# Optimization experiments

Hardware: AMD Instinct MI355X
Metric: run time of the kernel (lower is better)

The kernel has to match this reference:

```python
import jax, jax.numpy as jnp
import numpy as np

L, B, E = 8192, 2, 1024
H, WS = 16, 256
D = E // H


def setup_inputs() -> dict:
    key = jax.random.key(0)
    ks = jax.random.split(key, 8)
    mk = lambda k: jax.random.normal(k, (E, E), dtype=jnp.float32) * 0.02
    return {
        'query': jax.random.normal(ks[0], (L, B, E), dtype=jnp.float32),
        'key':   jax.random.normal(ks[1], (L, B, E), dtype=jnp.float32),
        'value': jax.random.normal(ks[2], (L, B, E), dtype=jnp.float32),
        'Wq': mk(ks[3]), 'bq': jnp.zeros((E,), jnp.float32),
        'Wk': mk(ks[4]), 'bk': jnp.zeros((E,), jnp.float32),
        'Wv': mk(ks[5]), 'bv': jnp.zeros((E,), jnp.float32),
        'Wo': mk(ks[6]), 'bo': jnp.zeros((E,), jnp.float32),
    }


def reference(query, key, value, Wq, bq, Wk, bk, Wv, bv, Wo, bo):
    # Faithful translation, including the original's (B,L,H,D) layout and the
    # raw-memory view(B,H,L//ws,ws,D) reinterpretation of that layout.
    proj = lambda x, W, b: x @ W.T + b
    # (L,B,E) -> (L,B,H,D) -> transpose(0,1) -> (B,L,H,D)
    q = jnp.swapaxes(proj(query, Wq, bq).reshape(L, B, H, D), 0, 1)
    k = jnp.swapaxes(proj(key,   Wk, bk).reshape(L, B, H, D), 0, 1)
    v = jnp.swapaxes(proj(value, Wv, bv).reshape(L, B, H, D), 0, 1)
    # L > ws, L % ws == 0 -> pad_len = 0; contiguous().view == reshape
    nW = L // WS
    q = q.reshape(B, H, nW, WS, D)
    k = k.reshape(B, H, nW, WS, D)
    v = v.reshape(B, H, nW, WS, D)
    attn = jnp.einsum('bhnqd,bhnkd->bhnqk', q, k) / (D ** 0.5)
    attn = jax.nn.softmax(attn, axis=-1)
    out = jnp.einsum('bhnqk,bhnkd->bhnqd', attn, v)  # (B,H,nW,ws,D)
    out = out.reshape(B, H, L, D)
    # transpose(0,1).contiguous().view(L,B,E): reinterpret (H,B,L,D) memory
    out = jnp.swapaxes(out, 0, 1).reshape(L, B, E)
    return out @ Wo.T + bo
```

## Files before the change

kernel.cpp:

```cpp
#include <hip/hip_runtime.h>


typedef _Float16 half8 __attribute__((ext_vector_type(8)));
typedef _Float16 half4 __attribute__((ext_vector_type(4)));
typedef float    f32x4 __attribute__((ext_vector_type(4)));

#define MFMA16(a, b, c) __builtin_amdgcn_mfma_f32_16x16x32_f16((a), (b), (c), 0, 0, 0)
#define VM(n) asm volatile("s_waitcnt vmcnt(" #n ")" ::: "memory")
#define SCHED0 __builtin_amdgcn_sched_barrier(0)
#define LGKM0 do { asm volatile("s_waitcnt lgkmcnt(0)" ::: "memory"); SCHED0; } while (0)
#define BARW do { __builtin_amdgcn_s_barrier(); SCHED0; } while (0)

__device__ inline void gload16(const _Float16* g, _Float16* l) {
  __builtin_amdgcn_global_load_lds(
      (const __attribute__((address_space(1))) void*)g,
      (__attribute__((address_space(3))) void*)l, 16, 0, 0);
}

__device__ inline half8 cvt8(float4 a, float4 b) {
  half8 h = {(_Float16)a.x, (_Float16)a.y, (_Float16)a.z, (_Float16)a.w,
             (_Float16)b.x, (_Float16)b.y, (_Float16)b.z, (_Float16)b.w};
  return h;
}

__global__ __launch_bounds__(256) void cvt_fp16_k(const float* __restrict__ src,
                                                  _Float16* __restrict__ dst, int n) {
  int i = (blockIdx.x * 256 + threadIdx.x) * 8;
  if (i >= n) return;
  float4 a = *(const float4*)(src + i);
  float4 b = *(const float4*)(src + i + 4);
  *(half8*)(dst + i) = cvt8(a, b);
}

__global__ __launch_bounds__(256) void cvtw_k(const float* __restrict__ s0,
                                              const float* __restrict__ s1,
                                              const float* __restrict__ s2,
                                              const float* __restrict__ s3,
                                              _Float16* __restrict__ d) {
  const float* s = blockIdx.y == 0 ? s0 : blockIdx.y == 1 ? s1 : blockIdx.y == 2 ? s2 : s3;
  _Float16* dst = d + (size_t)blockIdx.y * (1 << 20);
  int i = (blockIdx.x * 256 + threadIdx.x) * 8;
  float4 a = *(const float4*)(s + i);
  float4 b = *(const float4*)(s + i + 4);
  *(half8*)(dst + i) = cvt8(a, b);
}

template <int OUT_F32>
__global__ __launch_bounds__(512) void gemm8p_k(const _Float16* __restrict__ Ah,
                                                const _Float16* __restrict__ Bw,
                                                const float* __restrict__ bias,
                                                void* __restrict__ Cout, float scale) {
  constexpr int K = 1024, NN = 1024, NT = 16;
  __shared__ alignas(16) _Float16 SH[65536];
  const int tid = threadIdx.x, lane = tid & 63, wave = tid >> 6;
  const int r15 = lane & 15, g = lane >> 4;
  const int wr = wave >> 2, wc = wave & 3;
  const int m0 = blockIdx.x * 256, n0 = blockIdx.y * 256;

  const int sp = tid >> 3;
  const int sv = (tid & 7) ^ (sp & 7);
  const int srow = 2 * sp + (sv >> 2);
  const int scol = (sv & 3) * 8;
  const int sdst = tid * 8;

  const int rp = r15 >> 1, rsub = r15 & 1;
  const int rslot = ((rsub * 4 + g) ^ rp) * 8;

  f32x4 acc[8][4] = {};
  half8 af[4], bf[4];

#define A_REGION(buf, kh) (&SH[(buf)*16384 + (kh)*8192])
#define B_REGION(buf, kh) (&SH[32768 + (buf)*16384 + (kh)*8192])

#define STAGE_B(t, buf, kh)                                                    \
  do {                                                                         \
    const _Float16* _s = Bw + (size_t)(n0 + srow) * K + (t)*64 + (kh)*32 + scol; \
    gload16(_s, B_REGION(buf, kh) + sdst);                                     \
    gload16(_s + (size_t)128 * K, B_REGION(buf, kh) + sdst + 4096);            \
  } while (0)

#define STAGE_A16(t, buf, kh)                                                  \
  do {                                                                         \
    const _Float16* _s = Ah + (size_t)(m0 + srow) * K + (t)*64 + (kh)*32 + scol; \
    gload16(_s, A_REGION(buf, kh) + sdst);                                     \
    gload16(_s + (size_t)128 * K, A_REGION(buf, kh) + sdst + 4096);            \
  } while (0)

#define READ_AF(buf, kk, MH)                                                   \
  do {                                                                         \
    _Float16* _b = A_REGION(buf, kk);                                          \
    int _pb = (wr * 64 + (MH)*32 + rp) * 64 + rslot;                           \
    af[0] = *(half8*)&_b[_pb];                                                 \
    af[1] = *(half8*)&_b[_pb + 512];                                           \
    af[2] = *(half8*)&_b[_pb + 1024];                                          \
    af[3] = *(half8*)&_b[_pb + 1536];                                          \
  } while (0)

#define READ_BF(buf, kk)                                                       \
  do {                                                                         \
    _Float16* _b = B_REGION(buf, kk);                                          \
    int _pb = (wc * 32 + rp) * 64 + rslot;                                     \
    bf[0] = *(half8*)&_b[_pb];                                                 \
    bf[1] = *(half8*)&_b[_pb + 512];                                           \
    bf[2] = *(half8*)&_b[_pb + 1024];                                          \
    bf[3] = *(half8*)&_b[_pb + 1536];                                          \
  } while (0)

#define MFMA_Q(MH)                                                             \
  do {                                                                         \
    __builtin_amdgcn_s_setprio(1);                                             \
    _Pragma("unroll") for (int mi = 0; mi < 4; mi++)                           \
        _Pragma("unroll") for (int ni = 0; ni < 4; ni++) acc[(MH)*4 + mi][ni] = \
        MFMA16(af[mi], bf[ni], acc[(MH)*4 + mi][ni]);                          \
    __builtin_amdgcn_s_setprio(0);                                             \
  } while (0)

  STAGE_A16(0, 0, 0);
  STAGE_A16(0, 0, 1);
  STAGE_B(0, 0, 0);
  STAGE_B(0, 0, 1);

  for (int t = 0; t < NT - 1; t++) {
    const int buf = t & 1, nb = buf ^ 1;
    STAGE_A16(t + 1, nb, 0);
    VM(4);
    SCHED0; BARW;
    READ_AF(buf, 0, 0);
    READ_BF(buf, 0);
    LGKM0;
    MFMA_Q(0);
    STAGE_A16(t + 1, nb, 1);
    READ_AF(buf, 0, 1);
    LGKM0;
    MFMA_Q(1);
    STAGE_B(t + 1, nb, 0);
    VM(6);
    SCHED0; BARW;
    READ_AF(buf, 1, 0);
    READ_BF(buf, 1);
    LGKM0;
    MFMA_Q(0);
    STAGE_B(t + 1, nb, 1);
    READ_AF(buf, 1, 1);
    LGKM0;
    MFMA_Q(1);
  }
  {
    VM(2);
    SCHED0; BARW;
    READ_AF(1, 0, 0);
    READ_BF(1, 0);
    LGKM0;
    MFMA_Q(0);
    READ_AF(1, 0, 1);
    LGKM0;
    MFMA_Q(1);
    VM(0);
    SCHED0; BARW;
    READ_AF(1, 1, 0);
    READ_BF(1, 1);
    LGKM0;
    MFMA_Q(0);
    READ_AF(1, 1, 1);
    LGKM0;
    MFMA_Q(1);
  }

#pragma unroll
  for (int ni = 0; ni < 4; ni++) {
    const int col = n0 + wc * 64 + ni * 16 + r15;
    const float bv = bias[col];
#pragma unroll
    for (int mi8 = 0; mi8 < 8; mi8++) {
      const int rowb = m0 + wr * 128 + mi8 * 16 + g * 4;
#pragma unroll
      for (int r = 0; r < 4; r++) {
        float x = (acc[mi8][ni][r] + bv) * scale;
        if (OUT_F32)
          ((float*)Cout)[(size_t)(rowb + r) * NN + col] = x;
        else
          ((_Float16*)Cout)[(size_t)(rowb + r) * NN + col] = (_Float16)x;
      }
    }
  }
#undef A_REGION
#undef B_REGION
#undef STAGE_B
#undef STAGE_A16
#undef READ_AF
#undef READ_BF
#undef MFMA_Q
}

__global__ __launch_bounds__(256) void vtrans_k(const _Float16* __restrict__ Vp,
                                                _Float16* __restrict__ Vt) {
  const int c = blockIdx.x, b = blockIdx.y;
  __shared__ alignas(16) _Float16 Vl[256 * 64];
  const int tid = threadIdx.x;
  const int l0 = c * 16;
#pragma unroll
  for (int i = 0; i < 8; i++) {
    int q = tid + i * 256;
    int w = q >> 3, ck = q & 7;
    int ls = l0 + (w >> 4), h = w & 15;
    half8 v = *(const half8*)(Vp + (size_t)(ls * 2 + b) * 1024 + h * 64 + ck * 8);
    *(half8*)&Vl[w * 64 + (ck ^ (w & 7)) * 8] = v;
  }
  __syncthreads();
  const int d = tid >> 2, kcq = tid & 3;
  const size_t obase = ((size_t)(b * 512 + c) * 64 + d) * 256 + kcq * 64;
#pragma unroll
  for (int i8 = 0; i8 < 8; i8++) {
    half8 v;
#pragma unroll
    for (int j = 0; j < 8; j++) {
      int k = kcq * 64 + i8 * 8 + j;
      v[j] = Vl[k * 64 + (((d >> 3) ^ (k & 7)) * 8) + (d & 7)];
    }
    *(half8*)(Vt + obase + i8 * 8) = v;
  }
}

__global__ __launch_bounds__(512) void attn_win_k(const _Float16* __restrict__ Qp,
                                                  const _Float16* __restrict__ Kp,
                                                  const _Float16* __restrict__ Vt,
                                                  _Float16* __restrict__ Y) {
  const int c = blockIdx.x, b = blockIdx.y;
  __shared__ alignas(16) _Float16 Kl[256 * 64];
  __shared__ alignas(16) _Float16 Vl[64 * 256];
  const int tid = threadIdx.x, lane = tid & 63, wave = tid >> 6;
  const int i15 = lane & 15, g = lane >> 4;
  const int l0 = c * 16;

#pragma unroll
  for (int i = 0; i < 4; i++) {
    int q = tid + i * 512;
    int w = q >> 3, ck = q & 7;
    int ls = l0 + (w >> 4), h = w & 15;
    half8 v = *(const half8*)(Kp + (size_t)(ls * 2 + b) * 1024 + h * 64 + ck * 8);
    *(half8*)&Kl[w * 64 + (ck ^ (w & 7)) * 8] = v;
  }
  const size_t vb0 = (size_t)(b * 512 + c) * 64 * 256;
#pragma unroll
  for (int i = 0; i < 4; i++) {
    int q = tid + i * 512;
    int d = q >> 5, ck = q & 31;
    half8 v = *(const half8*)(Vt + vb0 + (size_t)d * 256 + ck * 8);
    *(half8*)&Vl[d * 256 + (ck ^ ((d & 7) << 2)) * 8] = v;
  }
  half8 qf[2][2];
#pragma unroll
  for (int wf = 0; wf < 2; wf++)
#pragma unroll
    for (int dh = 0; dh < 2; dh++) {
      int ls = l0 + wave * 2 + wf;
      qf[wf][dh] =
          *(const half8*)(Qp + (size_t)(ls * 2 + b) * 1024 + i15 * 64 + dh * 32 + g * 8);
    }
  __syncthreads();

  f32x4 acc[16][2] = {};
#pragma unroll
  for (int m = 0; m < 16; m++) {
    int row = m * 16 + i15;
    half8 a0 = *(half8*)&Kl[row * 64 + ((g) ^ (i15 & 7)) * 8];
    half8 a1 = *(half8*)&Kl[row * 64 + ((4 + g) ^ (i15 & 7)) * 8];
    __builtin_amdgcn_s_setprio(1);
    acc[m][0] = MFMA16(a0, qf[0][0], acc[m][0]);
    acc[m][0] = MFMA16(a1, qf[0][1], acc[m][0]);
    acc[m][1] = MFMA16(a0, qf[1][0], acc[m][1]);
    acc[m][1] = MFMA16(a1, qf[1][1], acc[m][1]);
    __builtin_amdgcn_s_setprio(0);
  }

  float inv[2];
#pragma unroll
  for (int wf = 0; wf < 2; wf++) {
    f32x4 t[8];
#pragma unroll
    for (int i = 0; i < 8; i++) {
#pragma unroll
      for (int c4 = 0; c4 < 4; c4++)
        t[i][c4] = fmaxf(acc[i][wf][c4], acc[i + 8][wf][c4]);
    }
#pragma unroll
    for (int i = 0; i < 4; i++)
#pragma unroll
      for (int c4 = 0; c4 < 4; c4++) t[i][c4] = fmaxf(t[i][c4], t[i + 4][c4]);
#pragma unroll
    for (int i = 0; i < 2; i++)
#pragma unroll
      for (int c4 = 0; c4 < 4; c4++) t[i][c4] = fmaxf(t[i][c4], t[i + 2][c4]);
#pragma unroll
    for (int c4 = 0; c4 < 4; c4++) t[0][c4] = fmaxf(t[0][c4], t[1][c4]);
    float mx = fmaxf(fmaxf(t[0][0], t[0][1]), fmaxf(t[0][2], t[0][3]));
    mx = fmaxf(mx, __shfl_xor(mx, 16, 64));
    mx = fmaxf(mx, __shfl_xor(mx, 32, 64));
    f32x4 s4 = {0.f, 0.f, 0.f, 0.f};
#pragma unroll
    for (int m = 0; m < 16; m++) {
#pragma unroll
      for (int c4 = 0; c4 < 4; c4++) {
        float e = __builtin_amdgcn_exp2f(acc[m][wf][c4] - mx);
        acc[m][wf][c4] = e;
        s4[c4] += e;
      }
    }
    float sum = (s4[0] + s4[1]) + (s4[2] + s4[3]);
    sum += __shfl_xor(sum, 16, 64);
    sum += __shfl_xor(sum, 32, 64);
    inv[wf] = 1.f / sum;
  }
  float invv[2][4];
#pragma unroll
  for (int wf = 0; wf < 2; wf++)
#pragma unroll
    for (int r = 0; r < 4; r++) invv[wf][r] = __shfl(inv[wf], g * 4 + r, 64);
  __syncthreads();

  _Float16* Pw = &Kl[wave * 2048];
  f32x4 oacc[2][4] = {};
#pragma unroll
  for (int kq = 0; kq < 4; kq++) {
#pragma unroll
    for (int wf = 0; wf < 2; wf++) {
      int rrow = wf * 16 + i15;
#pragma unroll
      for (int ml = 0; ml < 4; ml++) {
        f32x4 pv = acc[kq * 4 + ml][wf];
        half4 h = {(_Float16)pv[0], (_Float16)pv[1], (_Float16)pv[2], (_Float16)pv[3]};
        int ck = ml * 2 + (g >> 1);
        *(half4*)&Pw[rrow * 64 + ((ck ^ (i15 & 7)) * 8) + (g & 1) * 4] = h;
      }
    }
    asm volatile("s_waitcnt lgkmcnt(0)" ::: "memory");
    __builtin_amdgcn_sched_barrier(0);
#pragma unroll
    for (int kfl = 0; kfl < 2; kfl++) {
      half8 pa0 = *(half8*)&Pw[(i15)*64 + (((kfl * 4 + g) ^ (i15 & 7)) * 8)];
      half8 pa1 = *(half8*)&Pw[(16 + i15) * 64 + (((kfl * 4 + g) ^ (i15 & 7)) * 8)];
      __builtin_amdgcn_s_setprio(1);
#pragma unroll
      for (int df = 0; df < 4; df++) {
        int drow = df * 16 + i15;
        half8 vbf =
            *(half8*)&Vl[drow * 256 + (((kq * 8 + kfl * 4 + g) ^ ((i15 & 7) << 2)) * 8)];
        oacc[0][df] = MFMA16(pa0, vbf, oacc[0][df]);
        oacc[1][df] = MFMA16(pa1, vbf, oacc[1][df]);
      }
      __builtin_amdgcn_s_setprio(0);
    }
  }

  const int h2 = c >> 5, n = c & 31;
  const size_t yb = ((size_t)(h2 * 2 + b) * 8192 + (size_t)n * 256) * 64;
#pragma unroll
  for (int wf = 0; wf < 2; wf++)
#pragma unroll
    for (int df = 0; df < 4; df++)
#pragma unroll
      for (int r = 0; r < 4; r++) {
        int w = wave * 32 + wf * 16 + g * 4 + r;
        Y[yb + (size_t)w * 64 + df * 16 + i15] =
            (_Float16)(oacc[wf][df][r] * invv[wf][r]);
      }
}

extern "C" void kernel_launch(void* const* d_in, const int* in_sizes, int n_in,
                              void* d_out, int out_size, void* d_ws, size_t ws_size,
                              hipStream_t stream) {
  const float* query = (const float*)d_in[0];
  const float* key_ = (const float*)d_in[1];
  const float* value = (const float*)d_in[2];
  const float* Wq = (const float*)d_in[3];
  const float* bq = (const float*)d_in[4];
  const float* Wk = (const float*)d_in[5];
  const float* bk = (const float*)d_in[6];
  const float* Wv = (const float*)d_in[7];
  const float* bv = (const float*)d_in[8];
  const float* Wo = (const float*)d_in[9];
  const float* bo = (const float*)d_in[10];

  _Float16* ws = (_Float16*)d_ws;
  _Float16* W16 = ws;
  _Float16* W16q = W16;
  _Float16* W16k = W16 + (1 << 20);
  _Float16* W16v = W16 + 2 * (1 << 20);
  _Float16* W16o = W16 + 3 * (1 << 20);
  _Float16* X16 = ws + 4 * (1 << 20);
  _Float16* Vp = X16 + (1 << 24);
  _Float16* Vt = X16;
  _Float16* Ybuf = Vp;

  _Float16* Qp = (_Float16*)d_out;
  _Float16* Kp = Qp + (1 << 24);

  const float qscale = 0.125f * 1.44269504f;

  cvtw_k<<<dim3(512, 4), 256, 0, stream>>>(Wq, Wk, Wv, Wo, W16);

  dim3 gg(64, 4), gb(512);

  cvt_fp16_k<<<8192, 256, 0, stream>>>(query, X16, 1 << 24);
  gemm8p_k<0><<<gg, gb, 0, stream>>>(X16, W16q, bq, (void*)Qp, qscale);

  cvt_fp16_k<<<8192, 256, 0, stream>>>(key_, X16, 1 << 24);
  gemm8p_k<0><<<gg, gb, 0, stream>>>(X16, W16k, bk, (void*)Kp, 1.0f);

  cvt_fp16_k<<<8192, 256, 0, stream>>>(value, X16, 1 << 24);
  gemm8p_k<0><<<gg, gb, 0, stream>>>(X16, W16v, bv, (void*)Vp, 1.0f);

  vtrans_k<<<dim3(512, 2), 256, 0, stream>>>(Vp, Vt);
  attn_win_k<<<dim3(512, 2), 512, 0, stream>>>(Qp, Kp, Vt, Ybuf);

  gemm8p_k<1><<<gg, gb, 0, stream>>>(Ybuf, W16o, bo, d_out, 1.0f);

  (void)in_sizes; (void)n_in; (void)out_size; (void)ws_size;
}
```

Before: 274.1 us.

## Split attention block across z and read K/V directly from global memory

The window-attention kernel no longer stages K and V tiles in LDS. Each wave loads its K and V MFMA fragments straight from global memory, and LDS holds only the per-wave P buffer. The block is halved to 256 threads across a new grid z dimension, which removes the block-wide barriers and the large LDS footprint so more blocks can be resident. In exchange each half-block re-reads the same K/V window from global or L2, doubling that traffic and exposing global load latency inside the MFMA loops.

```diff
diff --git a/kernel.cpp b/kernel.cpp
--- a/kernel.cpp
+++ b/kernel.cpp
@@ -221,50 +221,33 @@
   }
 }
 
-__global__ __launch_bounds__(512) void attn_win_k(const _Float16* __restrict__ Qp,
+__global__ __launch_bounds__(256) void attn_win_k(const _Float16* __restrict__ Qp,
                                                   const _Float16* __restrict__ Kp,
                                                   const _Float16* __restrict__ Vt,
                                                   _Float16* __restrict__ Y) {
-  const int c = blockIdx.x, b = blockIdx.y;
-  __shared__ alignas(16) _Float16 Kl[256 * 64];
-  __shared__ alignas(16) _Float16 Vl[64 * 256];
+  const int c = blockIdx.x, b = blockIdx.y, hf = blockIdx.z;
+  __shared__ alignas(16) _Float16 Pl[4 * 2048];
   const int tid = threadIdx.x, lane = tid & 63, wave = tid >> 6;
   const int i15 = lane & 15, g = lane >> 4;
   const int l0 = c * 16;
-
-#pragma unroll
-  for (int i = 0; i < 4; i++) {
-    int q = tid + i * 512;
-    int w = q >> 3, ck = q & 7;
-    int ls = l0 + (w >> 4), h = w & 15;
-    half8 v = *(const half8*)(Kp + (size_t)(ls * 2 + b) * 1024 + h * 64 + ck * 8);
-    *(half8*)&Kl[w * 64 + (ck ^ (w & 7)) * 8] = v;
-  }
-  const size_t vb0 = (size_t)(b * 512 + c) * 64 * 256;
-#pragma unroll
-  for (int i = 0; i < 4; i++) {
-    int q = tid + i * 512;
-    int d = q >> 5, ck = q & 31;
-    half8 v = *(const half8*)(Vt + vb0 + (size_t)d * 256 + ck * 8);
-    *(half8*)&Vl[d * 256 + (ck ^ ((d & 7) << 2)) * 8] = v;
-  }
+  const int wv = hf * 4 + wave;
+
   half8 qf[2][2];
 #pragma unroll
   for (int wf = 0; wf < 2; wf++)
 #pragma unroll
     for (int dh = 0; dh < 2; dh++) {
-      int ls = l0 + wave * 2 + wf;
+      int ls = l0 + wv * 2 + wf;
       qf[wf][dh] =
           *(const half8*)(Qp + (size_t)(ls * 2 + b) * 1024 + i15 * 64 + dh * 32 + g * 8);
     }
-  __syncthreads();
 
   f32x4 acc[16][2] = {};
 #pragma unroll
   for (int m = 0; m < 16; m++) {
-    int row = m * 16 + i15;
-    half8 a0 = *(half8*)&Kl[row * 64 + ((g) ^ (i15 & 7)) * 8];
-    half8 a1 = *(half8*)&Kl[row * 64 + ((4 + g) ^ (i15 & 7)) * 8];
+    const _Float16* kb = Kp + (size_t)((l0 + m) * 2 + b) * 1024 + i15 * 64 + g * 8;
+    half8 a0 = *(const half8*)kb;
+    half8 a1 = *(const half8*)(kb + 32);
     __builtin_amdgcn_s_setprio(1);
     acc[m][0] = MFMA16(a0, qf[0][0], acc[m][0]);
     acc[m][0] = MFMA16(a1, qf[0][1], acc[m][0]);
@@ -316,9 +299,9 @@
   for (int wf = 0; wf < 2; wf++)
 #pragma unroll
     for (int r = 0; r < 4; r++) invv[wf][r] = __shfl(inv[wf], g * 4 + r, 64);
-  __syncthreads();
-
-  _Float16* Pw = &Kl[wave * 2048];
+
+  _Float16* Pw = &Pl[wave * 2048];
+  const size_t vb0 = (size_t)(b * 512 + c) * 64 * 256;
   f32x4 oacc[2][4] = {};
 #pragma unroll
   for (int kq = 0; kq < 4; kq++) {
@@ -339,16 +322,15 @@
     for (int kfl = 0; kfl < 2; kfl++) {
       half8 pa0 = *(half8*)&Pw[(i15)*64 + (((kfl * 4 + g) ^ (i15 & 7)) * 8)];
       half8 pa1 = *(half8*)&Pw[(16 + i15) * 64 + (((kfl * 4 + g) ^ (i15 & 7)) * 8)];
-      __builtin_amdgcn_s_setprio(1);
 #pragma unroll
       for (int df = 0; df < 4; df++) {
-        int drow = df * 16 + i15;
-        half8 vbf =
-            *(half8*)&Vl[drow * 256 + (((kq * 8 + kfl * 4 + g) ^ ((i15 & 7) << 2)) * 8)];
+        half8 vbf = *(const half8*)(Vt + vb0 + (size_t)(df * 16 + i15) * 256 +
+                                    (kq * 8 + kfl * 4 + g) * 8);
+        __builtin_amdgcn_s_setprio(1);
         oacc[0][df] = MFMA16(pa0, vbf, oacc[0][df]);
         oacc[1][df] = MFMA16(pa1, vbf, oacc[1][df]);
+        __builtin_amdgcn_s_setprio(0);
       }
-      __builtin_amdgcn_s_setprio(0);
     }
   }
 
@@ -360,7 +342,7 @@
     for (int df = 0; df < 4; df++)
 #pragma unroll
       for (int r = 0; r < 4; r++) {
-        int w = wave * 32 + wf * 16 + g * 4 + r;
+        int w = wv * 32 + wf * 16 + g * 4 + r;
         Y[yb + (size_t)w * 64 + df * 16 + i15] =
             (_Float16)(oacc[wf][df][r] * invv[wf][r]);
       }
@@ -411,7 +393,7 @@
   gemm8p_k<0><<<gg, gb, 0, stream>>>(X16, W16v, bv, (void*)Vp, 1.0f);
 
   vtrans_k<<<dim3(512, 2), 256, 0, stream>>>(Vp, Vt);
-  attn_win_k<<<dim3(512, 2), 512, 0, stream>>>(Qp, Kp, Vt, Ybuf);
+  attn_win_k<<<dim3(512, 2, 2), 256, 0, stream>>>(Qp, Kp, Vt, Ybuf);
 
   gemm8p_k<1><<<gg, gb, 0, stream>>>(Ybuf, W16o, bo, d_out, 1.0f);
 
```

Result: slower. 346.8 us (+26.5%).
